# Performance work log

Hardware: AMD Instinct MI355X
Metric: run time of the kernel (lower is better)

## Reference

```python
import jax, jax.numpy as jnp
import numpy as np

B, N, M = 2, 2048, 2048
D = 1024          # query_dim == context_dim == inner_dim
H, DH = 16, 64    # heads, dim_head
SCALE = DH ** -0.5


def setup_inputs() -> dict:
    key = jax.random.key(0)
    ks = jax.random.split(key, 7)
    s = 0.02
    return {
        "x": jax.random.normal(ks[0], (B, N, D), jnp.float32),
        "context": jax.random.normal(ks[1], (B, M, D), jnp.float32),
        "Wq": jax.random.normal(ks[2], (D, H * DH), jnp.float32) * s,
        "Wk": jax.random.normal(ks[3], (D, H * DH), jnp.float32) * s,
        "Wv": jax.random.normal(ks[4], (D, H * DH), jnp.float32) * s,
        "Wo": jax.random.normal(ks[5], (H * DH, D), jnp.float32) * s,
        "bo": jax.random.normal(ks[6], (D,), jnp.float32) * s,
    }


def reference(x, context, Wq, Wk, Wv, Wo, bo):
    # Linear projections (bias-free, as in to_q/to_k/to_v)
    q = (x @ Wq).reshape(B, N, H, DH)        # [B,N,H,DH]
    k = (context @ Wk).reshape(B, M, H, DH)  # [B,M,H,DH]
    v = (context @ Wv).reshape(B, M, H, DH)
    # QK^T * scale, softmax over keys, then AV
    sim = jnp.einsum('bnhd,bmhd->bhnm', q, k) * SCALE  # [B,H,N,M]
    attn = jax.nn.softmax(sim, axis=-1)
    out = jnp.einsum('bhnm,bmhd->bnhd', attn, v)       # [B,N,H,DH]
    out = out.reshape(B, N, H * DH)
    return out @ Wo + bo  # to_out Linear; dropout=0 is identity
```

## Files before the change

### kernel.cpp

```cpp
#include <hip/hip_runtime.h>

#define B_  2
#define N_  2048
#define M_  2048
#define D_  1024
#define H_  16
#define DH_ 64

typedef __bf16 bf16x8 __attribute__((ext_vector_type(8)));
typedef __bf16 bf16x4 __attribute__((ext_vector_type(4)));
typedef short  short4v __attribute__((ext_vector_type(4)));
typedef float  f32x4  __attribute__((ext_vector_type(4)));

#define GAS(p) ((__attribute__((address_space(1))) void*)(p))
#define LAS(p) ((__attribute__((address_space(3))) void*)(p))

#define QPRESCALE 0.18033688011112042f

__device__ __forceinline__ unsigned short f2bf(float f) {
    unsigned int u = __builtin_bit_cast(unsigned int, f);
    u += 0x7fffu + ((u >> 16) & 1u);
    return (unsigned short)(u >> 16);
}

__global__ __launch_bounds__(256) void prep(
    const float* __restrict__ x, const float* __restrict__ ctx,
    const float* __restrict__ Wq, const float* __restrict__ Wk,
    const float* __restrict__ Wv, const float* __restrict__ Wo,
    unsigned short* __restrict__ xb, unsigned short* __restrict__ cb,
    unsigned short* __restrict__ WTbase)
{
    if (blockIdx.z == 4) {
        int blk = blockIdx.y * 32 + blockIdx.x;
        int stride = 1024 * 256;
        for (int i = blk * 256 + threadIdx.x; i < 2097152; i += stride) {
            const float4* src; unsigned short* dst; int j;
            if (i < 1048576) { src = (const float4*)x;   dst = xb; j = i; }
            else             { src = (const float4*)ctx; dst = cb; j = i - 1048576; }
            float4 v = src[j];
            ushort4 o = make_ushort4(f2bf(v.x), f2bf(v.y), f2bf(v.z), f2bf(v.w));
            *(ushort4*)(dst + 4*j) = o;
        }
        return;
    }
    const float* W = (blockIdx.z == 0) ? Wq : (blockIdx.z == 1) ? Wk
                    : (blockIdx.z == 2) ? Wv : Wo;
    unsigned short* WT = WTbase + (size_t)blockIdx.z * 1048576;
    __shared__ unsigned short t[32][33];
    int tx = threadIdx.x & 31, ty8 = threadIdx.x >> 5;
    int c = blockIdx.x * 32 + tx;
#pragma unroll
    for (int i = 0; i < 4; ++i) {
        int r = blockIdx.y * 32 + i*8 + ty8;
        t[i*8 + ty8][tx] = f2bf(W[(size_t)r * 1024 + c]);
    }
    __syncthreads();
    int c2 = blockIdx.y * 32 + tx;
#pragma unroll
    for (int i = 0; i < 4; ++i) {
        int r2 = blockIdx.x * 32 + i*8 + ty8;
        WT[(size_t)r2 * 1024 + c2] = t[tx][i*8 + ty8];
    }
}

__global__ __launch_bounds__(256) void gemm128(
    const unsigned short* __restrict__ xb,
    const unsigned short* __restrict__ cb,
    const unsigned short* __restrict__ wT,
    const unsigned short* __restrict__ aoA,
    unsigned short* __restrict__ qkv_out,
    const float* __restrict__ bo,
    float* __restrict__ outF,
    int base_mode)
{
    __shared__ __align__(16) unsigned short As[128*32];
    __shared__ __align__(16) unsigned short Bs[128*32];

    const int mode = base_mode + blockIdx.z;
    const unsigned short* Amat = (mode == 0) ? xb : (mode == 3) ? aoA : cb;
    const unsigned short* Bt = wT + (size_t)mode * 1048576;

    const int tid = threadIdx.x;
    const int w = tid >> 6, l = tid & 63;
    const int quad = l >> 4, l16 = l & 15;
    const int wm = w & 1, wn = w >> 1;
    const int row0 = blockIdx.y * 128, col0 = blockIdx.x * 128;

    f32x4 acc[4][4];
#pragma unroll
    for (int i = 0; i < 4; ++i)
#pragma unroll
        for (int j = 0; j < 4; ++j) acc[i][j] = (f32x4){0.f, 0.f, 0.f, 0.f};

    for (int k0 = 0; k0 < 1024; k0 += 32) {
        __syncthreads();
#pragma unroll
        for (int i = 0; i < 2; ++i) {
            int s = i*256 + w*64 + l;
            int m = s >> 2, c = s & 3;
            int cs = c ^ ((m >> 1) & 3);
            __builtin_amdgcn_global_load_lds(
                GAS(Amat + (size_t)(row0 + m)*1024 + k0 + cs*8),
                LAS(As + (i*256 + w*64)*8), 16, 0, 0);
            __builtin_amdgcn_global_load_lds(
                GAS(Bt + (size_t)(col0 + m)*1024 + k0 + cs*8),
                LAS(Bs + (i*256 + w*64)*8), 16, 0, 0);
        }
        __syncthreads();

        bf16x8 af[4], bfr[4];
#pragma unroll
        for (int mt = 0; mt < 4; ++mt) {
            int m = wm*64 + mt*16 + l16;
            af[mt] = *reinterpret_cast<const bf16x8*>(As + m*32 + (quad ^ ((m >> 1) & 3))*8);
            int n = wn*64 + mt*16 + l16;
            bfr[mt] = *reinterpret_cast<const bf16x8*>(Bs + n*32 + (quad ^ ((n >> 1) & 3))*8);
        }
#pragma unroll
        for (int mt = 0; mt < 4; ++mt)
#pragma unroll
            for (int nt = 0; nt < 4; ++nt)
                acc[mt][nt] = __builtin_amdgcn_mfma_f32_16x16x32_bf16(
                    af[mt], bfr[nt], acc[mt][nt], 0, 0, 0);
    }

    if (mode == 3) {
#pragma unroll
        for (int nt = 0; nt < 4; ++nt) {
            int col = col0 + wn*64 + nt*16 + l16;
            float bv = bo[col];
#pragma unroll
            for (int mt = 0; mt < 4; ++mt) {
                int gr = row0 + wm*64 + mt*16 + quad*4;
#pragma unroll
                for (int r = 0; r < 4; ++r)
                    outF[(size_t)(gr + r)*1024 + col] = acc[mt][nt][r] + bv;
            }
        }
    } else if (mode == 2) {
#pragma unroll
        for (int mt = 0; mt < 4; ++mt) {
            int gr = row0 + wm*64 + mt*16 + quad*4;
            int b = gr >> 11, nidx = gr & 2047;
#pragma unroll
            for (int nt = 0; nt < 4; ++nt) {
                int col = col0 + wn*64 + nt*16 + l16;
                int h = col >> 6, d = col & 63;
                ushort4 pk = make_ushort4(f2bf(acc[mt][nt][0]), f2bf(acc[mt][nt][1]),
                                          f2bf(acc[mt][nt][2]), f2bf(acc[mt][nt][3]));
                *(ushort4*)(qkv_out + (size_t)2*4194304
                            + (size_t)((b*16 + h)*64 + d)*2048 + nidx) = pk;
            }
        }
    } else {
        const float qs = (mode == 0) ? QPRESCALE : 1.0f;
#pragma unroll
        for (int mt = 0; mt < 4; ++mt) {
            int gr = row0 + wm*64 + mt*16 + quad*4;
#pragma unroll
            for (int nt = 0; nt < 4; ++nt) {
                int col = col0 + wn*64 + nt*16 + l16;
                int h = col >> 6, d = col & 63;
#pragma unroll
                for (int r = 0; r < 4; ++r) {
                    int grr = gr + r;
                    int b = grr >> 11, nidx = grr & 2047;
                    qkv_out[(size_t)mode*4194304
                            + (size_t)((b*16 + h)*2048 + nidx)*64 + d]
                        = f2bf(acc[mt][nt][r] * qs);
                }
            }
        }
    }
}

__global__ __launch_bounds__(256, 2) void flash_attn(
    const unsigned short* __restrict__ qw,
    const unsigned short* __restrict__ kw,
    const unsigned short* __restrict__ vtw,
    unsigned short* __restrict__ ao)
{
    __shared__ __align__(16) unsigned short Tile[2][9216];

    const int tid = threadIdx.x;
    const int w = tid >> 6, l = tid & 63;
    const int quad = l >> 4, l16 = l & 15;
    const int bh = blockIdx.z * H_ + blockIdx.y;
    const int q0 = blockIdx.x * 128 + w * 32;

    int goff[5];
#pragma unroll
    for (int i = 0; i < 5; ++i) {
        int n = i*256 + w*64 + l;
        int m = (n < 576) ? n : n - 576;
        int row = m / 9, c = m % 9;  if (c > 7) c = 7;
        goff[i] = (n < 576) ? row*64 + c*8 : row*2048 + c*8;
    }
    const unsigned short* kbase = kw + (size_t)bh*131072;
    const unsigned short* vbase = vtw + (size_t)bh*131072;

    bf16x8 qf[2][2];
#pragma unroll
    for (int qg = 0; qg < 2; ++qg)
#pragma unroll
        for (int s = 0; s < 2; ++s)
            qf[qg][s] = *reinterpret_cast<const bf16x8*>(
                qw + (size_t)(bh*2048 + q0 + qg*16 + l16)*64 + s*32 + quad*8);

    f32x4 accO[2][4];
#pragma unroll
    for (int qg = 0; qg < 2; ++qg)
#pragma unroll
        for (int td = 0; td < 4; ++td) accO[qg][td] = (f32x4){0.f, 0.f, 0.f, 0.f};
    float lpart[2] = {0.f, 0.f};

    const f32x4 zz = (f32x4){0.f, 0.f, 0.f, 0.f};

    {
#pragma unroll
        for (int i = 0; i < 4; ++i) {
            const unsigned short* bp = (i*4 + w < 9) ? kbase : vbase;
            __builtin_amdgcn_global_load_lds(GAS(bp + goff[i]),
                LAS(&Tile[0][(i*256 + w*64)*8]), 16, 0, 0);
        }
        if (w < 2)
            __builtin_amdgcn_global_load_lds(GAS(vbase + goff[4]),
                LAS(&Tile[0][(1024 + w*64)*8]), 16, 0, 0);
    }

    for (int it = 0; it < 32; ++it) {
        __syncthreads();
        const int cur = it & 1;

        if (it + 1 < 32) {
            const unsigned short* kp = kbase + (it+1)*4096;
            const unsigned short* vp = vbase + (it+1)*64;
#pragma unroll
            for (int i = 0; i < 4; ++i) {
                const unsigned short* bp = (i*4 + w < 9) ? kp : vp;
                __builtin_amdgcn_global_load_lds(GAS(bp + goff[i]),
                    LAS(&Tile[cur^1][(i*256 + w*64)*8]), 16, 0, 0);
            }
            if (w < 2)
                __builtin_amdgcn_global_load_lds(GAS(vp + goff[4]),
                    LAS(&Tile[cur^1][(1024 + w*64)*8]), 16, 0, 0);
        }

        const unsigned short* Ks = &Tile[cur][0];
        const unsigned short* Vs = &Tile[cur][4608];

        f32x4 sac[2][4];
#pragma unroll
        for (int t = 0; t < 4; ++t) {
            const unsigned short* krow = Ks + (t*16 + l16)*72 + quad*8;
            bf16x8 kf0 = *reinterpret_cast<const bf16x8*>(krow);
            bf16x8 kf1 = *reinterpret_cast<const bf16x8*>(krow + 32);
            sac[0][t] = __builtin_amdgcn_mfma_f32_16x16x32_bf16(kf0, qf[0][0], zz, 0, 0, 0);
            sac[1][t] = __builtin_amdgcn_mfma_f32_16x16x32_bf16(kf0, qf[1][0], zz, 0, 0, 0);
            sac[0][t] = __builtin_amdgcn_mfma_f32_16x16x32_bf16(kf1, qf[0][1], sac[0][t], 0, 0, 0);
            sac[1][t] = __builtin_amdgcn_mfma_f32_16x16x32_bf16(kf1, qf[1][1], sac[1][t], 0, 0, 0);
        }

        short4v pk[2][4];
#pragma unroll
        for (int qg = 0; qg < 2; ++qg) {
            float s0 = 0.f, s1 = 0.f, s2 = 0.f, s3 = 0.f;
#pragma unroll
            for (int t = 0; t < 4; ++t) {
                float p0 = __builtin_amdgcn_exp2f(sac[qg][t][0]);
                float p1 = __builtin_amdgcn_exp2f(sac[qg][t][1]);
                float p2 = __builtin_amdgcn_exp2f(sac[qg][t][2]);
                float p3 = __builtin_amdgcn_exp2f(sac[qg][t][3]);
                s0 += p0; s1 += p1; s2 += p2; s3 += p3;
                bf16x4 pb;
                pb[0] = (__bf16)p0; pb[1] = (__bf16)p1;
                pb[2] = (__bf16)p2; pb[3] = (__bf16)p3;
                pk[qg][t] = __builtin_bit_cast(short4v, pb);
            }
            lpart[qg] += (s0 + s1) + (s2 + s3);
        }

#pragma unroll
        for (int td = 0; td < 4; ++td) {
            const unsigned short* vrow = Vs + (td*16 + l16)*72 + quad*4;
#pragma unroll
            for (int t = 0; t < 4; ++t) {
                short4v vf = *reinterpret_cast<const short4v*>(vrow + t*16);
                accO[0][td] = __builtin_amdgcn_mfma_f32_16x16x16bf16_1k(
                    vf, pk[0][t], accO[0][td], 0, 0, 0);
                accO[1][td] = __builtin_amdgcn_mfma_f32_16x16x16bf16_1k(
                    vf, pk[1][t], accO[1][td], 0, 0, 0);
            }
        }
    }

#pragma unroll
    for (int qg = 0; qg < 2; ++qg) {
        float s = lpart[qg];
        s += __shfl_xor(s, 16);
        s += __shfl_xor(s, 32);
        float inv = 1.f / s;
        const size_t rowbase =
            (size_t)(blockIdx.z*2048 + q0 + qg*16 + l16)*1024 + blockIdx.y*64;
#pragma unroll
        for (int td = 0; td < 4; ++td)
#pragma unroll
            for (int r = 0; r < 4; ++r)
                ao[rowbase + td*16 + quad*4 + r] = f2bf(accO[qg][td][r] * inv);
    }
}

extern "C" void kernel_launch(void* const* d_in, const int* in_sizes, int n_in,
                              void* d_out, int out_size, void* d_ws, size_t ws_size,
                              hipStream_t stream)
{
    const float* x   = (const float*)d_in[0];
    const float* ctx = (const float*)d_in[1];
    const float* Wq  = (const float*)d_in[2];
    const float* Wk  = (const float*)d_in[3];
    const float* Wv  = (const float*)d_in[4];
    const float* Wo  = (const float*)d_in[5];
    const float* bo  = (const float*)d_in[6];
    float* out = (float*)d_out;

    unsigned short* ws  = (unsigned short*)d_ws;
    unsigned short* xb  = ws;
    unsigned short* cb  = ws + 4194304;
    unsigned short* wT  = ws + 8388608;
    unsigned short* qkv = ws + 12582912;
    unsigned short* ao  = ws;

    prep<<<dim3(32, 32, 5), dim3(256), 0, stream>>>(x, ctx, Wq, Wk, Wv, Wo, xb, cb, wT);
    gemm128<<<dim3(8, 32, 3), dim3(256), 0, stream>>>(xb, cb, wT, ao, qkv, bo, out, 0);
    flash_attn<<<dim3(16, 16, 2), dim3(256), 0, stream>>>(qkv, qkv + 4194304, qkv + 8388608, ao);
    gemm128<<<dim3(8, 32, 1), dim3(256), 0, stream>>>(xb, cb, wT, ao, qkv, bo, out, 3);
}
```

Before: 222.6 us.

## Halve queries per warp in flash attention to double grid occupancy

Each warp now handles one 16-row query group instead of two, so a block covers 64 queries and the grid doubles along x. Launch bounds rise to 4 blocks per SM, lowering register pressure to allow more resident waves. This is meant to improve latency hiding and CU fill. In exchange, every K/V tile staged in LDS is reused by half as many queries, doubling K/V global and LDS traffic per unit of work.

```diff
diff --git a/kernel.cpp b/kernel.cpp
--- a/kernel.cpp
+++ b/kernel.cpp
@@ -174,7 +174,7 @@
     }
 }
 
-__global__ __launch_bounds__(256, 2) void flash_attn(
+__global__ __launch_bounds__(256, 4) void flash_attn(
     const unsigned short* __restrict__ qw,
     const unsigned short* __restrict__ kw,
     const unsigned short* __restrict__ vtw,
@@ -186,7 +186,7 @@
     const int w = tid >> 6, l = tid & 63;
     const int quad = l >> 4, l16 = l & 15;
     const int bh = blockIdx.z * H_ + blockIdx.y;
-    const int q0 = blockIdx.x * 128 + w * 32;
+    const int q0 = blockIdx.x * 64 + w * 16;
 
     int goff[5];
 #pragma unroll
@@ -199,20 +199,16 @@
     const unsigned short* kbase = kw + (size_t)bh*131072;
     const unsigned short* vbase = vtw + (size_t)bh*131072;
 
-    bf16x8 qf[2][2];
-#pragma unroll
-    for (int qg = 0; qg < 2; ++qg)
-#pragma unroll
-        for (int s = 0; s < 2; ++s)
-            qf[qg][s] = *reinterpret_cast<const bf16x8*>(
-                qw + (size_t)(bh*2048 + q0 + qg*16 + l16)*64 + s*32 + quad*8);
-
-    f32x4 accO[2][4];
-#pragma unroll
-    for (int qg = 0; qg < 2; ++qg)
-#pragma unroll
-        for (int td = 0; td < 4; ++td) accO[qg][td] = (f32x4){0.f, 0.f, 0.f, 0.f};
-    float lpart[2] = {0.f, 0.f};
+    bf16x8 qf[2];
+#pragma unroll
+    for (int s = 0; s < 2; ++s)
+        qf[s] = *reinterpret_cast<const bf16x8*>(
+            qw + (size_t)(bh*2048 + q0 + l16)*64 + s*32 + quad*8);
+
+    f32x4 accO[4];
+#pragma unroll
+    for (int td = 0; td < 4; ++td) accO[td] = (f32x4){0.f, 0.f, 0.f, 0.f};
+    float lpart = 0.f;
 
     const f32x4 zz = (f32x4){0.f, 0.f, 0.f, 0.f};
 
@@ -249,35 +245,32 @@
         const unsigned short* Ks = &Tile[cur][0];
         const unsigned short* Vs = &Tile[cur][4608];
 
-        f32x4 sac[2][4];
+        f32x4 sac[4];
 #pragma unroll
         for (int t = 0; t < 4; ++t) {
             const unsigned short* krow = Ks + (t*16 + l16)*72 + quad*8;
             bf16x8 kf0 = *reinterpret_cast<const bf16x8*>(krow);
             bf16x8 kf1 = *reinterpret_cast<const bf16x8*>(krow + 32);
-            sac[0][t] = __builtin_amdgcn_mfma_f32_16x16x32_bf16(kf0, qf[0][0], zz, 0, 0, 0);
-            sac[1][t] = __builtin_amdgcn_mfma_f32_16x16x32_bf16(kf0, qf[1][0], zz, 0, 0, 0);
-            sac[0][t] = __builtin_amdgcn_mfma_f32_16x16x32_bf16(kf1, qf[0][1], sac[0][t], 0, 0, 0);
-            sac[1][t] = __builtin_amdgcn_mfma_f32_16x16x32_bf16(kf1, qf[1][1], sac[1][t], 0, 0, 0);
-        }
-
-        short4v pk[2][4];
-#pragma unroll
-        for (int qg = 0; qg < 2; ++qg) {
+            sac[t] = __builtin_amdgcn_mfma_f32_16x16x32_bf16(kf0, qf[0], zz, 0, 0, 0);
+            sac[t] = __builtin_amdgcn_mfma_f32_16x16x32_bf16(kf1, qf[1], sac[t], 0, 0, 0);
+        }
+
+        short4v pk[4];
+        {
             float s0 = 0.f, s1 = 0.f, s2 = 0.f, s3 = 0.f;
 #pragma unroll
             for (int t = 0; t < 4; ++t) {
-                float p0 = __builtin_amdgcn_exp2f(sac[qg][t][0]);
-                float p1 = __builtin_amdgcn_exp2f(sac[qg][t][1]);
-                float p2 = __builtin_amdgcn_exp2f(sac[qg][t][2]);
-                float p3 = __builtin_amdgcn_exp2f(sac[qg][t][3]);
+                float p0 = __builtin_amdgcn_exp2f(sac[t][0]);
+                float p1 = __builtin_amdgcn_exp2f(sac[t][1]);
+                float p2 = __builtin_amdgcn_exp2f(sac[t][2]);
+                float p3 = __builtin_amdgcn_exp2f(sac[t][3]);
                 s0 += p0; s1 += p1; s2 += p2; s3 += p3;
                 bf16x4 pb;
                 pb[0] = (__bf16)p0; pb[1] = (__bf16)p1;
                 pb[2] = (__bf16)p2; pb[3] = (__bf16)p3;
-                pk[qg][t] = __builtin_bit_cast(short4v, pb);
-            }
-            lpart[qg] += (s0 + s1) + (s2 + s3);
+                pk[t] = __builtin_bit_cast(short4v, pb);
+            }
+            lpart += (s0 + s1) + (s2 + s3);
         }
 
 #pragma unroll
@@ -286,27 +279,24 @@
 #pragma unroll
             for (int t = 0; t < 4; ++t) {
                 short4v vf = *reinterpret_cast<const short4v*>(vrow + t*16);
-                accO[0][td] = __builtin_amdgcn_mfma_f32_16x16x16bf16_1k(
-                    vf, pk[0][t], accO[0][td], 0, 0, 0);
-                accO[1][td] = __builtin_amdgcn_mfma_f32_16x16x16bf16_1k(
-                    vf, pk[1][t], accO[1][td], 0, 0, 0);
-            }
-        }
-    }
-
-#pragma unroll
-    for (int qg = 0; qg < 2; ++qg) {
-        float s = lpart[qg];
+                accO[td] = __builtin_amdgcn_mfma_f32_16x16x16bf16_1k(
+                    vf, pk[t], accO[td], 0, 0, 0);
+            }
+        }
+    }
+
+    {
+        float s = lpart;
         s += __shfl_xor(s, 16);
         s += __shfl_xor(s, 32);
         float inv = 1.f / s;
         const size_t rowbase =
-            (size_t)(blockIdx.z*2048 + q0 + qg*16 + l16)*1024 + blockIdx.y*64;
+            (size_t)(blockIdx.z*2048 + q0 + l16)*1024 + blockIdx.y*64;
 #pragma unroll
         for (int td = 0; td < 4; ++td)
 #pragma unroll
             for (int r = 0; r < 4; ++r)
-                ao[rowbase + td*16 + quad*4 + r] = f2bf(accO[qg][td][r] * inv);
+                ao[rowbase + td*16 + quad*4 + r] = f2bf(accO[td][r] * inv);
     }
 }
 
@@ -332,6 +322,6 @@
 
     prep<<<dim3(32, 32, 5), dim3(256), 0, stream>>>(x, ctx, Wq, Wk, Wv, Wo, xb, cb, wT);
     gemm128<<<dim3(8, 32, 3), dim3(256), 0, stream>>>(xb, cb, wT, ao, qkv, bo, out, 0);
-    flash_attn<<<dim3(16, 16, 2), dim3(256), 0, stream>>>(qkv, qkv + 4194304, qkv + 8388608, ao);
+    flash_attn<<<dim3(32, 16, 2), dim3(256), 0, stream>>>(qkv, qkv + 4194304, qkv + 8388608, ao);
     gemm128<<<dim3(8, 32, 1), dim3(256), 0, stream>>>(xb, cb, wT, ao, qkv, bo, out, 3);
 }
```

Measured after the change: 228.1 us. +2.5%, slower.

## Load K tiles directly into registers, keep only V in LDS

Applied to the files above, without the earlier changes.

K fragments are no longer staged through shared memory. Each wave loads its K fragments straight from global memory into double-buffered registers, prefetching the next tile while the current one is consumed, and only V^T stays in the LDS double buffer. This removes the LDS write/read traffic and the shared-memory footprint for K. The cost is that every wave reads the full K tile from global/L2 (4x redundancy per block) and register pressure rises by 16 bf16x8 values, which may hurt occupancy under launch_bounds(256,2).

```diff
diff --git a/kernel.cpp b/kernel.cpp
--- a/kernel.cpp
+++ b/kernel.cpp
@@ -180,7 +180,7 @@
     const unsigned short* __restrict__ vtw,
     unsigned short* __restrict__ ao)
 {
-    __shared__ __align__(16) unsigned short Tile[2][9216];
+    __shared__ __align__(16) unsigned short Vt[2][4608];
 
     const int tid = threadIdx.x;
     const int w = tid >> 6, l = tid & 63;
@@ -188,13 +188,12 @@
     const int bh = blockIdx.z * H_ + blockIdx.y;
     const int q0 = blockIdx.x * 128 + w * 32;
 
-    int goff[5];
-#pragma unroll
-    for (int i = 0; i < 5; ++i) {
+    int goff[3];
+#pragma unroll
+    for (int i = 0; i < 3; ++i) {
         int n = i*256 + w*64 + l;
-        int m = (n < 576) ? n : n - 576;
-        int row = m / 9, c = m % 9;  if (c > 7) c = 7;
-        goff[i] = (n < 576) ? row*64 + c*8 : row*2048 + c*8;
+        int row = n / 9, c = n % 9;  if (c > 7) c = 7;
+        goff[i] = row*2048 + c*8;
     }
     const unsigned short* kbase = kw + (size_t)bh*131072;
     const unsigned short* vbase = vtw + (size_t)bh*131072;
@@ -216,49 +215,61 @@
 
     const f32x4 zz = (f32x4){0.f, 0.f, 0.f, 0.f};
 
+    const int kfo = l16*64 + quad*8;
+    bf16x8 ka[8], kb[8];
+
     {
 #pragma unroll
-        for (int i = 0; i < 4; ++i) {
-            const unsigned short* bp = (i*4 + w < 9) ? kbase : vbase;
-            __builtin_amdgcn_global_load_lds(GAS(bp + goff[i]),
-                LAS(&Tile[0][(i*256 + w*64)*8]), 16, 0, 0);
-        }
-        if (w < 2)
-            __builtin_amdgcn_global_load_lds(GAS(vbase + goff[4]),
-                LAS(&Tile[0][(1024 + w*64)*8]), 16, 0, 0);
-    }
-
+        for (int i = 0; i < 2; ++i)
+            __builtin_amdgcn_global_load_lds(GAS(vbase + goff[i]),
+                LAS(&Vt[0][(i*256 + w*64)*8]), 16, 0, 0);
+        if (w == 0)
+            __builtin_amdgcn_global_load_lds(GAS(vbase + goff[2]),
+                LAS(&Vt[0][512*8]), 16, 0, 0);
+#pragma unroll
+        for (int t = 0; t < 4; ++t)
+#pragma unroll
+            for (int s = 0; s < 2; ++s)
+                ka[t*2+s] = *reinterpret_cast<const bf16x8*>(
+                    kbase + t*1024 + s*32 + kfo);
+    }
+
+#pragma unroll 2
     for (int it = 0; it < 32; ++it) {
+        const int cur = it & 1;
+        bf16x8* KU = (it & 1) ? kb : ka;
+        bf16x8* KP = (it & 1) ? ka : kb;
+
         __syncthreads();
-        const int cur = it & 1;
 
         if (it + 1 < 32) {
-            const unsigned short* kp = kbase + (it+1)*4096;
             const unsigned short* vp = vbase + (it+1)*64;
 #pragma unroll
-            for (int i = 0; i < 4; ++i) {
-                const unsigned short* bp = (i*4 + w < 9) ? kp : vp;
-                __builtin_amdgcn_global_load_lds(GAS(bp + goff[i]),
-                    LAS(&Tile[cur^1][(i*256 + w*64)*8]), 16, 0, 0);
-            }
-            if (w < 2)
-                __builtin_amdgcn_global_load_lds(GAS(vp + goff[4]),
-                    LAS(&Tile[cur^1][(1024 + w*64)*8]), 16, 0, 0);
-        }
-
-        const unsigned short* Ks = &Tile[cur][0];
-        const unsigned short* Vs = &Tile[cur][4608];
+            for (int i = 0; i < 2; ++i)
+                __builtin_amdgcn_global_load_lds(GAS(vp + goff[i]),
+                    LAS(&Vt[cur^1][(i*256 + w*64)*8]), 16, 0, 0);
+            if (w == 0)
+                __builtin_amdgcn_global_load_lds(GAS(vp + goff[2]),
+                    LAS(&Vt[cur^1][512*8]), 16, 0, 0);
+        }
 
         f32x4 sac[2][4];
 #pragma unroll
         for (int t = 0; t < 4; ++t) {
-            const unsigned short* krow = Ks + (t*16 + l16)*72 + quad*8;
-            bf16x8 kf0 = *reinterpret_cast<const bf16x8*>(krow);
-            bf16x8 kf1 = *reinterpret_cast<const bf16x8*>(krow + 32);
-            sac[0][t] = __builtin_amdgcn_mfma_f32_16x16x32_bf16(kf0, qf[0][0], zz, 0, 0, 0);
-            sac[1][t] = __builtin_amdgcn_mfma_f32_16x16x32_bf16(kf0, qf[1][0], zz, 0, 0, 0);
-            sac[0][t] = __builtin_amdgcn_mfma_f32_16x16x32_bf16(kf1, qf[0][1], sac[0][t], 0, 0, 0);
-            sac[1][t] = __builtin_amdgcn_mfma_f32_16x16x32_bf16(kf1, qf[1][1], sac[1][t], 0, 0, 0);
+            sac[0][t] = __builtin_amdgcn_mfma_f32_16x16x32_bf16(KU[t*2+0], qf[0][0], zz, 0, 0, 0);
+            sac[1][t] = __builtin_amdgcn_mfma_f32_16x16x32_bf16(KU[t*2+0], qf[1][0], zz, 0, 0, 0);
+            sac[0][t] = __builtin_amdgcn_mfma_f32_16x16x32_bf16(KU[t*2+1], qf[0][1], sac[0][t], 0, 0, 0);
+            sac[1][t] = __builtin_amdgcn_mfma_f32_16x16x32_bf16(KU[t*2+1], qf[1][1], sac[1][t], 0, 0, 0);
+        }
+
+        {
+            const unsigned short* kp = kbase + (((it+1) & 31))*4096;
+#pragma unroll
+            for (int t = 0; t < 4; ++t)
+#pragma unroll
+                for (int s = 0; s < 2; ++s)
+                    KP[t*2+s] = *reinterpret_cast<const bf16x8*>(
+                        kp + t*1024 + s*32 + kfo);
         }
 
         short4v pk[2][4];
@@ -282,7 +293,7 @@
 
 #pragma unroll
         for (int td = 0; td < 4; ++td) {
-            const unsigned short* vrow = Vs + (td*16 + l16)*72 + quad*4;
+            const unsigned short* vrow = &Vt[cur][(td*16 + l16)*72 + quad*4];
 #pragma unroll
             for (int t = 0; t < 4; ++t) {
                 short4v vf = *reinterpret_cast<const short4v*>(vrow + t*16);
```

Result: slower. 240.6 us (+8.1%).
